# Performance work log

Hardware: AMD Instinct MI355X
Metric: run time of the kernel (lower is better)

Reference implementation:

```python
import jax, jax.numpy as jnp
import numpy as np

B, S, D, H = 4, 2048, 1024, 16
HD = D // H  # head dim = 64
NEG = jnp.finfo(jnp.float32).min


def setup_inputs() -> dict:
    key = jax.random.key(0)
    ks = jax.random.split(key, 6)
    states = jax.random.normal(ks[0], (B, S, D), dtype=jnp.float32)
    # causal float mask, broadcastable over batch and heads
    mask = jnp.tril(jnp.ones((S, S), dtype=jnp.float32))[None, None, :, :]
    scale = 1.0 / np.sqrt(D)
    Wq = jax.random.normal(ks[1], (D, D), dtype=jnp.float32) * scale
    Wk = jax.random.normal(ks[2], (D, D), dtype=jnp.float32) * scale
    Wv = jax.random.normal(ks[3], (D, D), dtype=jnp.float32) * scale
    Wo = jax.random.normal(ks[4], (D, D), dtype=jnp.float32) * scale
    return {"states": states, "mask": mask, "Wq": Wq, "Wk": Wk, "Wv": Wv, "Wo": Wo}


def _split_heads(x):
    # [B,S,D] -> [B,H,S,HD]
    return x.reshape(B, S, H, HD).transpose(0, 2, 1, 3)


def reference(states, mask, Wq, Wk, Wv, Wo):
    q = _split_heads(states @ Wq)
    k = _split_heads(states @ Wk)
    v = _split_heads(states @ Wv)
    # scores [B,H,S,S], scaled by rsqrt(head_dim) as in the original
    alpha = jnp.einsum("bhqd,bhkd->bhqk", q, k) * (1.0 / jnp.sqrt(jnp.float32(HD)))
    alpha = alpha * mask + (1.0 - mask) * NEG
    alpha = jax.nn.softmax(alpha, axis=-1)
    ctx = jnp.einsum("bhqk,bhkd->bhqd", alpha, v)
    ctx = ctx.transpose(0, 2, 1, 3).reshape(B, S, D)  # concat heads
    return ctx @ Wo
```

## Files before the change

kernel.cpp:

```cpp
#include <hip/hip_runtime.h>
#include <hip/hip_bf16.h>

#define BB 4
#define SS 2048
#define DD 1024
#define HH 16
#define HDD 64
#define MM (BB*SS)

typedef __attribute__((ext_vector_type(8))) short short8;
typedef __attribute__((ext_vector_type(4))) float f32x4;
typedef __attribute__((ext_vector_type(4))) int int4v;
typedef __attribute__((ext_vector_type(4))) short bf16x4;

__device__ __forceinline__ ushort f2bf(float f) {
  union { float f; uint u; } v; v.f = f;
  uint u = v.u;
  uint r = (u + 0x7FFFu + ((u >> 16) & 1u)) >> 16;
  return (ushort)r;
}

__device__ __forceinline__ float exp2f_fast(float x) {
#if __has_builtin(__builtin_amdgcn_exp2f)
  return __builtin_amdgcn_exp2f(x);
#else
  float r; asm("v_exp_f32 %0, %1" : "=v"(r) : "v"(x)); return r;
#endif
}

__device__ __forceinline__ bf16x4 pack4bf(float a, float b, float c, float d) {
  union { __hip_bfloat162 h2[2]; bf16x4 s; } u;
  u.h2[0] = __float22bfloat162_rn(make_float2(a, b));
  u.h2[1] = __float22bfloat162_rn(make_float2(c, d));
  return u.s;
}

__device__ __forceinline__ f32x4 mfma16(bf16x4 a, bf16x4 b, f32x4 c) {
#if __has_builtin(__builtin_amdgcn_mfma_f32_16x16x16bf16_1k)
  return __builtin_amdgcn_mfma_f32_16x16x16bf16_1k(a, b, c, 0, 0, 0);
#else
  f32x4 d;
  asm volatile("s_nop 1\n\tv_mfma_f32_16x16x16_bf16 %0, %1, %2, %3\n\ts_nop 7\n\ts_nop 3"
               : "=v"(d) : "v"(a), "v"(b), "v"(c));
  return d;
#endif
}

__device__ __forceinline__ void gload16(void* lds, const void* g) {
  __builtin_amdgcn_global_load_lds((const __attribute__((address_space(1))) void*)g,
                                   (__attribute__((address_space(3))) void*)lds, 16, 0, 0);
}

__global__ __launch_bounds__(256) void k_convert(const float* __restrict__ in,
                                                 ushort* __restrict__ out, int n4) {
  int i = blockIdx.x * 256 + threadIdx.x;
  if (i >= n4) return;
  float4 v = ((const float4*)in)[i];
  uint lo = (uint)f2bf(v.x) | ((uint)f2bf(v.y) << 16);
  uint hi = (uint)f2bf(v.z) | ((uint)f2bf(v.w) << 16);
  ((uint2*)out)[i] = make_uint2(lo, hi);
}

__global__ __launch_bounds__(256) void k_transpose(const float* __restrict__ W0, const float* __restrict__ W1,
                                                   const float* __restrict__ W2, const float* __restrict__ W3,
                                                   ushort* __restrict__ T0, ushort* __restrict__ T1,
                                                   ushort* __restrict__ T2, ushort* __restrict__ T3) {
  __shared__ float t[32][33];
  const float* W; ushort* T;
  switch (blockIdx.z) {
    case 0: W = W0; T = T0; break;
    case 1: W = W1; T = T1; break;
    case 2: W = W2; T = T2; break;
    default: W = W3; T = T3; break;
  }
  float scale = (blockIdx.z == 0) ? 0.18033688011112042f : 1.0f;
  int tx = threadIdx.x, ty = threadIdx.y;
  int x = blockIdx.x * 32 + tx;
  int y0 = blockIdx.y * 32;
#pragma unroll
  for (int j = 0; j < 32; j += 8) t[ty + j][tx] = W[(y0 + ty + j) * DD + x];
  __syncthreads();
#pragma unroll
  for (int j = 0; j < 32; j += 8)
    T[(blockIdx.x * 32 + ty + j) * DD + y0 + tx] = f2bf(t[tx][ty + j] * scale);
}

__device__ __forceinline__ void gemm_tile(const ushort* __restrict__ Arow,
                                          const ushort* __restrict__ Brow,
                                          ushort* Al, ushort* Bl,
                                          f32x4 acc[4][4]) {
  int tid = threadIdx.x;
  int lane = tid & 63, w = tid >> 6;
  int wm = w >> 1, wn = w & 1;
  int lrow = lane & 15, lgrp = lane >> 4;
#pragma unroll
  for (int i = 0; i < 4; i++)
#pragma unroll
    for (int j = 0; j < 4; j++)
#pragma unroll
      for (int r = 0; r < 4; r++) acc[i][j][r] = 0.f;

  int srow = lane >> 2;
  int scolb = (lane & 3) * 16;
  const char* A8 = (const char*)Arow;
  const char* B8 = (const char*)Brow;

#pragma unroll
  for (int ii = 0; ii < 2; ii++) {
    int i = w * 2 + ii;
    gload16(Al + i * 512, A8 + (size_t)(i * 16 + srow) * (DD * 2) + scolb);
    gload16(Bl + i * 512, B8 + (size_t)(i * 16 + srow) * (DD * 2) + scolb);
  }
  __syncthreads();

  for (int kk = 0; kk < DD; kk += 32) {
    int cur = (kk >> 5) & 1;
    if (kk + 32 < DD) {
#pragma unroll
      for (int ii = 0; ii < 2; ii++) {
        int i = w * 2 + ii;
        gload16(Al + (cur ^ 1) * 4096 + i * 512,
                A8 + (size_t)(i * 16 + srow) * (DD * 2) + (kk + 32) * 2 + scolb);
        gload16(Bl + (cur ^ 1) * 4096 + i * 512,
                B8 + (size_t)(i * 16 + srow) * (DD * 2) + (kk + 32) * 2 + scolb);
      }
    }
    short8 a[4], b[4];
#pragma unroll
    for (int i = 0; i < 4; i++) a[i] = *(const short8*)&Al[cur * 4096 + (wm * 64 + i * 16 + lrow) * 32 + lgrp * 8];
#pragma unroll
    for (int j = 0; j < 4; j++) b[j] = *(const short8*)&Bl[cur * 4096 + (wn * 64 + j * 16 + lrow) * 32 + lgrp * 8];
#pragma unroll
    for (int i = 0; i < 4; i++)
#pragma unroll
      for (int j = 0; j < 4; j++)
        acc[i][j] = __builtin_amdgcn_mfma_f32_16x16x32_bf16(a[i], b[j], acc[i][j], 0, 0, 0);
    __syncthreads();
  }
}

__global__ __launch_bounds__(256) void k_qkv(const ushort* __restrict__ X,
                                             const ushort* __restrict__ Wqt,
                                             const ushort* __restrict__ Wkt,
                                             const ushort* __restrict__ Wvt,
                                             ushort* __restrict__ Q,
                                             ushort* __restrict__ K,
                                             ushort* __restrict__ Vt) {
  __shared__ ushort Al[2 * 4096];
  __shared__ ushort Bl[2 * 4096];
  const ushort* Wt;
  switch (blockIdx.z) {
    case 0: Wt = Wqt; break;
    case 1: Wt = Wkt; break;
    default: Wt = Wvt; break;
  }
  f32x4 acc[4][4];
  gemm_tile(X + (size_t)blockIdx.x * 128 * DD, Wt + (size_t)blockIdx.y * 128 * DD, Al, Bl, acc);
  int lane = threadIdx.x & 63, w = threadIdx.x >> 6;
  int wm = w >> 1, wn = w & 1, lrow = lane & 15, lgrp = lane >> 4;
  int m0 = blockIdx.x * 128 + wm * 64, n0 = blockIdx.y * 128 + wn * 64;
  if (blockIdx.z == 2) {
#pragma unroll
    for (int i = 0; i < 4; i++)
#pragma unroll
      for (int j = 0; j < 4; j++) {
        int row0 = m0 + i * 16 + lgrp * 4;
        int col = n0 + j * 16 + lrow;
        int b = row0 >> 11, s0 = row0 & 2047, h = col >> 6, hd = col & 63;
        bf16x4 s = pack4bf(acc[i][j][0], acc[i][j][1], acc[i][j][2], acc[i][j][3]);
        *(bf16x4*)(Vt + (((size_t)(b * HH + h) * HDD) + hd) * SS + s0) = s;
      }
  } else {
    ushort* Out = (blockIdx.z == 0) ? Q : K;
#pragma unroll
    for (int i = 0; i < 4; i++)
#pragma unroll
      for (int j = 0; j < 4; j++)
#pragma unroll
        for (int r = 0; r < 4; r++) {
          int row = m0 + i * 16 + lgrp * 4 + r;
          int col = n0 + j * 16 + lrow;
          int b = row >> 11, s = row & 2047, h = col >> 6, hd = col & 63;
          Out[(((size_t)(b * HH + h) * SS) + s) * HDD + hd] = f2bf(acc[i][j][r]);
        }
  }
}

#define QB2 64
#define KVB 64
#define NQT2 (SS / QB2)

__global__ __launch_bounds__(128) void k_attn(const ushort* __restrict__ Q,
                                              const ushort* __restrict__ K,
                                              const ushort* __restrict__ Vt,
                                              ushort* __restrict__ Ctx) {
  __shared__ ushort Kl[2][4096];
  __shared__ ushort Vl[2][4096];
  int bid = blockIdx.x;
  int xcd = bid & 7, slot = bid >> 3;
  int j = slot & 15;
  int bh = (slot >> 4) * 8 + xcd;
  int b = bh >> 4, h = bh & 15;
  int tid = threadIdx.x, lane = tid & 63, w = tid >> 6;
  int lrow = lane & 15, lgrp = lane >> 4;

  int srow = lane >> 3;
  int scolb = ((lane & 7) * 16) ^ (srow << 4);
  const char* K8 = (const char*)(K + (size_t)bh * SS * HDD);
  const char* V8 = (const char*)(Vt + (size_t)bh * HDD * SS);

  int kswz = (lrow & 7) << 3;
  int colE[2];
  colE[0] = (lgrp * 8) ^ kswz;
  colE[1] = (lgrp * 8 + 32) ^ kswz;

#pragma unroll
  for (int ph = 0; ph < 2; ph++) {
    int qx = ph == 0 ? (NQT2 - 1 - j) : j;
    int qb = qx * QB2;
    int qw0 = qb + w * 32;
    int ntk = qx + 1;

    short8 qf[2][2];
#pragma unroll
    for (int qt = 0; qt < 2; qt++)
#pragma unroll
      for (int c = 0; c < 2; c++)
        qf[qt][c] = *(const short8*)(Q + ((size_t)bh * SS + qb + w * 32 + qt * 16 + lrow) * HDD + lgrp * 8 + 32 * c);

    f32x4 o[2][4];
#pragma unroll
    for (int qt = 0; qt < 2; qt++)
#pragma unroll
      for (int nt = 0; nt < 4; nt++)
#pragma unroll
        for (int r = 0; r < 4; r++) o[qt][nt][r] = 0.f;
    float m_run[2] = {-1e30f, -1e30f}, l_run[2] = {0.f, 0.f};

#pragma unroll
    for (int ii = 0; ii < 4; ii++) {
      int i = w * 4 + ii;
      gload16(&Kl[0][i * 512], K8 + (size_t)(i * 8 + srow) * 128 + scolb);
      gload16(&Vl[0][i * 512], V8 + (size_t)(i * 8 + srow) * (SS * 2) + scolb);
    }
    __syncthreads();

    for (int kt = 0; kt < ntk; kt++) {
      int cur = kt & 1;
      if (kt + 1 < ntk) {
        int kb2 = (kt + 1) * KVB;
#pragma unroll
        for (int ii = 0; ii < 4; ii++) {
          int i = w * 4 + ii;
          gload16(&Kl[cur ^ 1][i * 512], K8 + (size_t)(kb2 + i * 8 + srow) * 128 + scolb);
          gload16(&Vl[cur ^ 1][i * 512], V8 + (size_t)(i * 8 + srow) * (SS * 2) + (size_t)kb2 * 2 + scolb);
        }
      }
      int kb = kt * KVB;
      short8 kf[4][2];
#pragma unroll
      for (int t = 0; t < 4; t++)
#pragma unroll
        for (int c = 0; c < 2; c++)
          kf[t][c] = *(const short8*)&Kl[cur][(16 * t + lrow) * 64 + colE[c]];

      bf16x4 pk[2][4];
#pragma unroll
      for (int qt = 0; qt < 2; qt++) {
        f32x4 st[4];
#pragma unroll
        for (int t = 0; t < 4; t++) {
          f32x4 z;
#pragma unroll
          for (int r = 0; r < 4; r++) z[r] = 0.f;
          z = __builtin_amdgcn_mfma_f32_16x16x32_bf16(kf[t][0], qf[qt][0], z, 0, 0, 0);
          z = __builtin_amdgcn_mfma_f32_16x16x32_bf16(kf[t][1], qf[qt][1], z, 0, 0, 0);
          st[t] = z;
        }
        if (kb + 63 > qw0) {
          int lim = qw0 + qt * 16 + lrow - kb - lgrp * 4;
#pragma unroll
          for (int t = 0; t < 4; t++)
#pragma unroll
            for (int r = 0; r < 4; r++)
              if (16 * t + r > lim) st[t][r] = -1e30f;
        }
        float rm = -1e30f;
#pragma unroll
        for (int t = 0; t < 4; t++) {
          float m01 = fmaxf(st[t][0], st[t][1]);
          float m23 = fmaxf(st[t][2], st[t][3]);
          rm = fmaxf(rm, fmaxf(m01, m23));
        }
        rm = fmaxf(rm, __shfl_xor(rm, 16));
        rm = fmaxf(rm, __shfl_xor(rm, 32));
        bool need = rm > m_run[qt] + 8.f;
        if (__any(need)) {
          float mn = need ? rm : m_run[qt];
          float sca = exp2f_fast(m_run[qt] - mn);
          m_run[qt] = mn;
          l_run[qt] *= sca;
#pragma unroll
          for (int nt = 0; nt < 4; nt++)
#pragma unroll
            for (int r = 0; r < 4; r++) o[qt][nt][r] *= sca;
        }
        float m = m_run[qt];
        float rs = 0.f;
#pragma unroll
        for (int t = 0; t < 4; t++) {
          float e0 = exp2f_fast(st[t][0] - m);
          float e1 = exp2f_fast(st[t][1] - m);
          float e2 = exp2f_fast(st[t][2] - m);
          float e3 = exp2f_fast(st[t][3] - m);
          rs += (e0 + e1) + (e2 + e3);
          pk[qt][t] = pack4bf(e0, e1, e2, e3);
        }
        rs += __shfl_xor(rs, 16);
        rs += __shfl_xor(rs, 32);
        l_run[qt] += rs;
      }

#pragma unroll
      for (int nt = 0; nt < 4; nt++) {
#pragma unroll
        for (int t = 0; t < 4; t++) {
          bf16x4 va = *(const bf16x4*)&Vl[cur][(nt * 16 + lrow) * 64 + ((16 * t + lgrp * 4) ^ kswz)];
          o[0][nt] = mfma16(va, pk[0][t], o[0][nt]);
          o[1][nt] = mfma16(va, pk[1][t], o[1][nt]);
        }
      }
      __syncthreads();
    }

#pragma unroll
    for (int qt = 0; qt < 2; qt++) {
      float inv = 1.f / l_run[qt];
      int q = qb + w * 32 + qt * 16 + lrow;
      ushort* base = Ctx + ((size_t)b * SS + q) * DD + h * HDD;
#pragma unroll
      for (int nt = 0; nt < 4; nt++) {
        bf16x4 s = pack4bf(o[qt][nt][0] * inv, o[qt][nt][1] * inv,
                           o[qt][nt][2] * inv, o[qt][nt][3] * inv);
        *(bf16x4*)(base + nt * 16 + lgrp * 4) = s;
      }
    }
  }
}

__global__ __launch_bounds__(256) void k_oproj(const ushort* __restrict__ Ctx,
                                               const ushort* __restrict__ Wot,
                                               float* __restrict__ Outp) {
  __shared__ ushort Al[2 * 4096];
  __shared__ ushort Bl[2 * 4096];
  f32x4 acc[4][4];
  gemm_tile(Ctx + (size_t)blockIdx.x * 128 * DD, Wot + (size_t)blockIdx.y * 128 * DD, Al, Bl, acc);
  int lane = threadIdx.x & 63, w = threadIdx.x >> 6;
  int wm = w >> 1, wn = w & 1, lrow = lane & 15, lgrp = lane >> 4;
  int m0 = blockIdx.x * 128 + wm * 64, n0 = blockIdx.y * 128 + wn * 64;
#pragma unroll
  for (int i = 0; i < 4; i++)
#pragma unroll
    for (int j = 0; j < 4; j++)
#pragma unroll
      for (int r = 0; r < 4; r++) {
        int row = m0 + i * 16 + lgrp * 4 + r;
        int col = n0 + j * 16 + lrow;
        Outp[(size_t)row * DD + col] = acc[i][j][r];
      }
}

extern "C" void kernel_launch(void* const* d_in, const int* in_sizes, int n_in,
                              void* d_out, int out_size, void* d_ws, size_t ws_size,
                              hipStream_t stream) {
  const float* states = (const float*)d_in[0];
  const float* Wq = (const float*)d_in[2];
  const float* Wk = (const float*)d_in[3];
  const float* Wv = (const float*)d_in[4];
  const float* Wo = (const float*)d_in[5];
  float* outp = (float*)d_out;

  char* ws = (char*)d_ws;
  const size_t XBF = 0;
  const size_t WQT = 16777216;
  const size_t WKT = WQT + 2097152;
  const size_t WVT = WKT + 2097152;
  const size_t WOT = WVT + 2097152;
  const size_t QO  = WOT + 2097152;
  const size_t KO  = QO + 16777216;
  const size_t VT  = KO + 16777216;
  const size_t CTX = VT + 16777216;

  ushort* Xbf = (ushort*)(ws + XBF);
  ushort* Wqt = (ushort*)(ws + WQT);
  ushort* Wkt = (ushort*)(ws + WKT);
  ushort* Wvt = (ushort*)(ws + WVT);
  ushort* Wot = (ushort*)(ws + WOT);
  ushort* Qb  = (ushort*)(ws + QO);
  ushort* Kb  = (ushort*)(ws + KO);
  ushort* Vtb = (ushort*)(ws + VT);
  ushort* Ctb = (ushort*)(ws + CTX);

  k_convert<<<(MM * DD / 4 + 255) / 256, 256, 0, stream>>>(states, Xbf, MM * DD / 4);
  k_transpose<<<dim3(32, 32, 4), dim3(32, 8), 0, stream>>>(Wq, Wk, Wv, Wo, Wqt, Wkt, Wvt, Wot);
  k_qkv<<<dim3(MM / 128, DD / 128, 3), 256, 0, stream>>>(Xbf, Wqt, Wkt, Wvt, Qb, Kb, Vtb);
  k_attn<<<dim3(NQT2 * BB * HH / 2), 128, 0, stream>>>(Qb, Kb, Vtb, Ctb);
  k_oproj<<<dim3(MM / 128, DD / 128), 256, 0, stream>>>(Ctb, Wot, outp);
}
```

Measured before the change: 187.2 us.

## Fuse Q/K/V projections into one GEMM sharing the activation tile

```diff
diff --git a/kernel.cpp b/kernel.cpp
--- a/kernel.cpp
+++ b/kernel.cpp
@@ -85,31 +85,41 @@
     T[(blockIdx.x * 32 + ty + j) * DD + y0 + tx] = f2bf(t[tx][ty + j] * scale);
 }
 
-__device__ __forceinline__ void gemm_tile(const ushort* __restrict__ Arow,
-                                          const ushort* __restrict__ Brow,
-                                          ushort* Al, ushort* Bl,
-                                          f32x4 acc[4][4]) {
-  int tid = threadIdx.x;
-  int lane = tid & 63, w = tid >> 6;
-  int wm = w >> 1, wn = w & 1;
-  int lrow = lane & 15, lgrp = lane >> 4;
-#pragma unroll
-  for (int i = 0; i < 4; i++)
-#pragma unroll
-    for (int j = 0; j < 4; j++)
-#pragma unroll
-      for (int r = 0; r < 4; r++) acc[i][j][r] = 0.f;
-
-  int srow = lane >> 2;
-  int scolb = (lane & 3) * 16;
-  const char* A8 = (const char*)Arow;
-  const char* B8 = (const char*)Brow;
+__global__ __launch_bounds__(256, 2) void k_qkv(const ushort* __restrict__ X,
+                                                const ushort* __restrict__ Wqt,
+                                                const ushort* __restrict__ Wkt,
+                                                const ushort* __restrict__ Wvt,
+                                                ushort* __restrict__ Q,
+                                                ushort* __restrict__ K,
+                                                ushort* __restrict__ Vt) {
+  __shared__ ushort Al[2 * 4096];
+  __shared__ ushort Bl[3][2 * 4096];
+  int tid = threadIdx.x, lane = tid & 63, w = tid >> 6;
+  int wm = w >> 1, wn = w & 1, lrow = lane & 15, lgrp = lane >> 4;
+  int srow = lane >> 2, scolb = (lane & 3) * 16;
+  const char* A8 = (const char*)(X + (size_t)blockIdx.x * 128 * DD);
+  const char* B8[3] = { (const char*)(Wqt + (size_t)blockIdx.y * 128 * DD),
+                        (const char*)(Wkt + (size_t)blockIdx.y * 128 * DD),
+                        (const char*)(Wvt + (size_t)blockIdx.y * 128 * DD) };
+
+  f32x4 acc[3][4][4];
+#pragma unroll
+  for (int wi = 0; wi < 3; wi++)
+#pragma unroll
+    for (int i = 0; i < 4; i++)
+#pragma unroll
+      for (int j = 0; j < 4; j++)
+#pragma unroll
+        for (int r = 0; r < 4; r++) acc[wi][i][j][r] = 0.f;
 
 #pragma unroll
   for (int ii = 0; ii < 2; ii++) {
     int i = w * 2 + ii;
-    gload16(Al + i * 512, A8 + (size_t)(i * 16 + srow) * (DD * 2) + scolb);
-    gload16(Bl + i * 512, B8 + (size_t)(i * 16 + srow) * (DD * 2) + scolb);
+    size_t ro = (size_t)(i * 16 + srow) * (DD * 2) + scolb;
+    gload16(Al + i * 512, A8 + ro);
+#pragma unroll
+    for (int wi = 0; wi < 3; wi++)
+      gload16(&Bl[wi][i * 512], B8[wi] + ro);
   }
   __syncthreads();
 
@@ -119,59 +129,36 @@
 #pragma unroll
       for (int ii = 0; ii < 2; ii++) {
         int i = w * 2 + ii;
-        gload16(Al + (cur ^ 1) * 4096 + i * 512,
-                A8 + (size_t)(i * 16 + srow) * (DD * 2) + (kk + 32) * 2 + scolb);
-        gload16(Bl + (cur ^ 1) * 4096 + i * 512,
-                B8 + (size_t)(i * 16 + srow) * (DD * 2) + (kk + 32) * 2 + scolb);
-      }
-    }
-    short8 a[4], b[4];
-#pragma unroll
-    for (int i = 0; i < 4; i++) a[i] = *(const short8*)&Al[cur * 4096 + (wm * 64 + i * 16 + lrow) * 32 + lgrp * 8];
-#pragma unroll
-    for (int j = 0; j < 4; j++) b[j] = *(const short8*)&Bl[cur * 4096 + (wn * 64 + j * 16 + lrow) * 32 + lgrp * 8];
+        size_t ro = (size_t)(i * 16 + srow) * (DD * 2) + (kk + 32) * 2 + scolb;
+        gload16(Al + (cur ^ 1) * 4096 + i * 512, A8 + ro);
+#pragma unroll
+        for (int wi = 0; wi < 3; wi++)
+          gload16(&Bl[wi][(cur ^ 1) * 4096 + i * 512], B8[wi] + ro);
+      }
+    }
+    short8 a[4];
 #pragma unroll
     for (int i = 0; i < 4; i++)
+      a[i] = *(const short8*)&Al[cur * 4096 + (wm * 64 + i * 16 + lrow) * 32 + lgrp * 8];
+#pragma unroll
+    for (int wi = 0; wi < 3; wi++) {
+      short8 b[4];
 #pragma unroll
       for (int j = 0; j < 4; j++)
-        acc[i][j] = __builtin_amdgcn_mfma_f32_16x16x32_bf16(a[i], b[j], acc[i][j], 0, 0, 0);
+        b[j] = *(const short8*)&Bl[wi][cur * 4096 + (wn * 64 + j * 16 + lrow) * 32 + lgrp * 8];
+#pragma unroll
+      for (int i = 0; i < 4; i++)
+#pragma unroll
+        for (int j = 0; j < 4; j++)
+          acc[wi][i][j] = __builtin_amdgcn_mfma_f32_16x16x32_bf16(a[i], b[j], acc[wi][i][j], 0, 0, 0);
+    }
     __syncthreads();
   }
-}
-
-__global__ __launch_bounds__(256) void k_qkv(const ushort* __restrict__ X,
-                                             const ushort* __restrict__ Wqt,
-                                             const ushort* __restrict__ Wkt,
-                                             const ushort* __restrict__ Wvt,
-                                             ushort* __restrict__ Q,
-                                             ushort* __restrict__ K,
-                                             ushort* __restrict__ Vt) {
-  __shared__ ushort Al[2 * 4096];
-  __shared__ ushort Bl[2 * 4096];
-  const ushort* Wt;
-  switch (blockIdx.z) {
-    case 0: Wt = Wqt; break;
-    case 1: Wt = Wkt; break;
-    default: Wt = Wvt; break;
-  }
-  f32x4 acc[4][4];
-  gemm_tile(X + (size_t)blockIdx.x * 128 * DD, Wt + (size_t)blockIdx.y * 128 * DD, Al, Bl, acc);
-  int lane = threadIdx.x & 63, w = threadIdx.x >> 6;
-  int wm = w >> 1, wn = w & 1, lrow = lane & 15, lgrp = lane >> 4;
+
   int m0 = blockIdx.x * 128 + wm * 64, n0 = blockIdx.y * 128 + wn * 64;
-  if (blockIdx.z == 2) {
-#pragma unroll
-    for (int i = 0; i < 4; i++)
-#pragma unroll
-      for (int j = 0; j < 4; j++) {
-        int row0 = m0 + i * 16 + lgrp * 4;
-        int col = n0 + j * 16 + lrow;
-        int b = row0 >> 11, s0 = row0 & 2047, h = col >> 6, hd = col & 63;
-        bf16x4 s = pack4bf(acc[i][j][0], acc[i][j][1], acc[i][j][2], acc[i][j][3]);
-        *(bf16x4*)(Vt + (((size_t)(b * HH + h) * HDD) + hd) * SS + s0) = s;
-      }
-  } else {
-    ushort* Out = (blockIdx.z == 0) ? Q : K;
+#pragma unroll
+  for (int wi = 0; wi < 2; wi++) {
+    ushort* Out = (wi == 0) ? Q : K;
 #pragma unroll
     for (int i = 0; i < 4; i++)
 #pragma unroll
@@ -181,9 +168,19 @@
           int row = m0 + i * 16 + lgrp * 4 + r;
           int col = n0 + j * 16 + lrow;
           int b = row >> 11, s = row & 2047, h = col >> 6, hd = col & 63;
-          Out[(((size_t)(b * HH + h) * SS) + s) * HDD + hd] = f2bf(acc[i][j][r]);
-        }
-  }
+          Out[(((size_t)(b * HH + h) * SS) + s) * HDD + hd] = f2bf(acc[wi][i][j][r]);
+        }
+  }
+#pragma unroll
+  for (int i = 0; i < 4; i++)
+#pragma unroll
+    for (int j = 0; j < 4; j++) {
+      int row0 = m0 + i * 16 + lgrp * 4;
+      int col = n0 + j * 16 + lrow;
+      int b = row0 >> 11, s0 = row0 & 2047, h = col >> 6, hd = col & 63;
+      bf16x4 s = pack4bf(acc[2][i][j][0], acc[2][i][j][1], acc[2][i][j][2], acc[2][i][j][3]);
+      *(bf16x4*)(Vt + (((size_t)(b * HH + h) * HDD) + hd) * SS + s0) = s;
+    }
 }
 
 #define QB2 64
@@ -214,6 +211,12 @@
   colE[0] = (lgrp * 8) ^ kswz;
   colE[1] = (lgrp * 8 + 32) ^ kswz;
 
+  const ushort* kc0 = &Kl[0][lrow * 64 + colE[0]];
+  const ushort* kc1 = &Kl[0][lrow * 64 + colE[1]];
+  const ushort* vbp[4];
+#pragma unroll
+  for (int t = 0; t < 4; t++) vbp[t] = &Vl[0][lrow * 64 + (((16 * t + lgrp * 4) ^ kswz))];
+
 #pragma unroll
   for (int ph = 0; ph < 2; ph++) {
     int qx = ph == 0 ? (NQT2 - 1 - j) : j;
@@ -221,6 +224,14 @@
     int qw0 = qb + w * 32;
     int ntk = qx + 1;
 
+    const char* kgp[4];
+    const char* vgp[4];
+#pragma unroll
+    for (int ii = 0; ii < 4; ii++) {
+      kgp[ii] = K8 + (size_t)(w * 32 + ii * 8 + srow) * 128 + scolb;
+      vgp[ii] = V8 + (size_t)(w * 32 + ii * 8 + srow) * (SS * 2) + scolb;
+    }
+
     short8 qf[2][2];
 #pragma unroll
     for (int qt = 0; qt < 2; qt++)
@@ -239,30 +250,33 @@
 
 #pragma unroll
     for (int ii = 0; ii < 4; ii++) {
-      int i = w * 4 + ii;
-      gload16(&Kl[0][i * 512], K8 + (size_t)(i * 8 + srow) * 128 + scolb);
-      gload16(&Vl[0][i * 512], V8 + (size_t)(i * 8 + srow) * (SS * 2) + scolb);
+      gload16(&Kl[0][(w * 4 + ii) * 512], kgp[ii]);
+      gload16(&Vl[0][(w * 4 + ii) * 512], vgp[ii]);
+      kgp[ii] += KVB * 128;
+      vgp[ii] += KVB * 2;
     }
     __syncthreads();
 
     for (int kt = 0; kt < ntk; kt++) {
       int cur = kt & 1;
       if (kt + 1 < ntk) {
-        int kb2 = (kt + 1) * KVB;
 #pragma unroll
         for (int ii = 0; ii < 4; ii++) {
-          int i = w * 4 + ii;
-          gload16(&Kl[cur ^ 1][i * 512], K8 + (size_t)(kb2 + i * 8 + srow) * 128 + scolb);
-          gload16(&Vl[cur ^ 1][i * 512], V8 + (size_t)(i * 8 + srow) * (SS * 2) + (size_t)kb2 * 2 + scolb);
+          gload16(&Kl[cur ^ 1][(w * 4 + ii) * 512], kgp[ii]);
+          gload16(&Vl[cur ^ 1][(w * 4 + ii) * 512], vgp[ii]);
+          kgp[ii] += KVB * 128;
+          vgp[ii] += KVB * 2;
         }
       }
       int kb = kt * KVB;
+      const ushort* kcc0 = kc0 + (cur << 12);
+      const ushort* kcc1 = kc1 + (cur << 12);
       short8 kf[4][2];
 #pragma unroll
-      for (int t = 0; t < 4; t++)
-#pragma unroll
-        for (int c = 0; c < 2; c++)
-          kf[t][c] = *(const short8*)&Kl[cur][(16 * t + lrow) * 64 + colE[c]];
+      for (int t = 0; t < 4; t++) {
+        kf[t][0] = *(const short8*)(kcc0 + t * 1024);
+        kf[t][1] = *(const short8*)(kcc1 + t * 1024);
+      }
 
       bf16x4 pk[2][4];
 #pragma unroll
@@ -322,10 +336,11 @@
       }
 
 #pragma unroll
-      for (int nt = 0; nt < 4; nt++) {
-#pragma unroll
-        for (int t = 0; t < 4; t++) {
-          bf16x4 va = *(const bf16x4*)&Vl[cur][(nt * 16 + lrow) * 64 + ((16 * t + lgrp * 4) ^ kswz)];
+      for (int t = 0; t < 4; t++) {
+        const ushort* vbt = vbp[t] + (cur << 12);
+#pragma unroll
+        for (int nt = 0; nt < 4; nt++) {
+          bf16x4 va = *(const bf16x4*)(vbt + nt * 1024);
           o[0][nt] = mfma16(va, pk[0][t], o[0][nt]);
           o[1][nt] = mfma16(va, pk[1][t], o[1][nt]);
         }
@@ -345,6 +360,60 @@
         *(bf16x4*)(base + nt * 16 + lgrp * 4) = s;
       }
     }
+  }
+}
+
+__device__ __forceinline__ void gemm_tile(const ushort* __restrict__ Arow,
+                                          const ushort* __restrict__ Brow,
+                                          ushort* Al, ushort* Bl,
+                                          f32x4 acc[4][4]) {
+  int tid = threadIdx.x;
+  int lane = tid & 63, w = tid >> 6;
+  int wm = w >> 1, wn = w & 1;
+  int lrow = lane & 15, lgrp = lane >> 4;
+#pragma unroll
+  for (int i = 0; i < 4; i++)
+#pragma unroll
+    for (int j = 0; j < 4; j++)
+#pragma unroll
+      for (int r = 0; r < 4; r++) acc[i][j][r] = 0.f;
+
+  int srow = lane >> 2;
+  int scolb = (lane & 3) * 16;
+  const char* A8 = (const char*)Arow;
+  const char* B8 = (const char*)Brow;
+
+#pragma unroll
+  for (int ii = 0; ii < 2; ii++) {
+    int i = w * 2 + ii;
+    gload16(Al + i * 512, A8 + (size_t)(i * 16 + srow) * (DD * 2) + scolb);
+    gload16(Bl + i * 512, B8 + (size_t)(i * 16 + srow) * (DD * 2) + scolb);
+  }
+  __syncthreads();
+
+  for (int kk = 0; kk < DD; kk += 32) {
+    int cur = (kk >> 5) & 1;
+    if (kk + 32 < DD) {
+#pragma unroll
+      for (int ii = 0; ii < 2; ii++) {
+        int i = w * 2 + ii;
+        gload16(Al + (cur ^ 1) * 4096 + i * 512,
+                A8 + (size_t)(i * 16 + srow) * (DD * 2) + (kk + 32) * 2 + scolb);
+        gload16(Bl + (cur ^ 1) * 4096 + i * 512,
+                B8 + (size_t)(i * 16 + srow) * (DD * 2) + (kk + 32) * 2 + scolb);
+      }
+    }
+    short8 a[4], b[4];
+#pragma unroll
+    for (int i = 0; i < 4; i++) a[i] = *(const short8*)&Al[cur * 4096 + (wm * 64 + i * 16 + lrow) * 32 + lgrp * 8];
+#pragma unroll
+    for (int j = 0; j < 4; j++) b[j] = *(const short8*)&Bl[cur * 4096 + (wn * 64 + j * 16 + lrow) * 32 + lgrp * 8];
+#pragma unroll
+    for (int i = 0; i < 4; i++)
+#pragma unroll
+      for (int j = 0; j < 4; j++)
+        acc[i][j] = __builtin_amdgcn_mfma_f32_16x16x32_bf16(a[i], b[j], acc[i][j], 0, 0, 0);
+    __syncthreads();
   }
 }
 
@@ -403,7 +472,7 @@
 
   k_convert<<<(MM * DD / 4 + 255) / 256, 256, 0, stream>>>(states, Xbf, MM * DD / 4);
   k_transpose<<<dim3(32, 32, 4), dim3(32, 8), 0, stream>>>(Wq, Wk, Wv, Wo, Wqt, Wkt, Wvt, Wot);
-  k_qkv<<<dim3(MM / 128, DD / 128, 3), 256, 0, stream>>>(Xbf, Wqt, Wkt, Wvt, Qb, Kb, Vtb);
+  k_qkv<<<dim3(MM / 128, DD / 128), 256, 0, stream>>>(Xbf, Wqt, Wkt, Wvt, Qb, Kb, Vtb);
   k_attn<<<dim3(NQT2 * BB * HH / 2), 128, 0, stream>>>(Qb, Kb, Vtb, Ctb);
   k_oproj<<<dim3(MM / 128, DD / 128), 256, 0, stream>>>(Ctb, Wot, outp);
 }
```

Result: faster. 172.4 us (-7.9%).
